# Optimization experiments

Hardware: AMD Instinct MI355X
Metric: run time of the kernel (lower is better)

Reference implementation:

```python
import jax, jax.numpy as jnp
import numpy as np

# ---- configuration (matches init_kwargs) ----
S = 128          # sheet_units
AK = 21          # aff_cf_units
AC = 2           # aff_cf_channels
AD = 1           # aff_cf_dilation
LK = 41          # lat_cf_units
LD = 1           # lat_cf_dilation
EX = 9           # exc_units
ITERS = 5        # lat_iters
STRENGTH = 1.5
MAX_INH = 1.0
MAX_R = 19       # oddenise(2*exc_units)


def _dist(size):
    c = (size - 1) / 2.0
    r = jnp.arange(size, dtype=jnp.float32) - c
    return jnp.sqrt(r[:, None] ** 2 + r[None, :] ** 2)


def get_circle(size, radius):
    return (_dist(size) < radius).astype(jnp.float32)


def get_radial_cos(size, period):
    return jnp.cos(_dist(size) * jnp.pi / period)


def unfold(x, k, dil=1):
    # x: (N,C,H,W) -> (N, C*k*k, L); channel-major patch order (same as torch F.unfold)
    p = jax.lax.conv_general_dilated_patches(
        x, (k, k), (1, 1), 'VALID', rhs_dilation=(dil, dil))
    return p.reshape(p.shape[0], p.shape[1], -1)


def setup_inputs() -> dict:
    key = jax.random.key(0)
    k1, k2, k3 = jax.random.split(key, 3)
    # afferent receptive-field envelope
    env = get_radial_cos(AK, AK) ** 2 * get_circle(AK, AK / 2)
    env = env / env.max()
    aff_cf_envelope = jnp.tile(env[None, None], (1, AC, 1, 1)).reshape(1, AC * AK * AK, 1)
    # short-range excitation kernel (normalised to sum 1)
    sre = get_radial_cos(EX, EX) ** 2 * get_circle(EX, EX / 2)
    sre = (sre / sre.sum())[None, None]  # (1,1,EX,EX)
    # lateral-inhibition envelope (annulus: full cutoff minus excitatory core)
    inh_mask = get_radial_cos(LK, EX / LD) ** 2 * get_circle(LK, EX / (2 * LD))
    lri = get_radial_cos(LK, LK) ** 2 * get_circle(LK, LK / 2) * (1.0 - inh_mask)
    lri_envelope = lri.reshape(1, LK * LK, 1)
    lri_envelope = lri_envelope / lri_envelope.max()
    # circular mask for the masked max-pool
    max_mask = get_circle(MAX_R, MAX_R / 2).reshape(1, MAX_R * MAX_R, 1)
    # parameters (init as in the module, jittered so they are not degenerate)
    P = AC * AK * AK
    K = LK * LK
    rfs = jnp.ones((S * S, P, 1), jnp.float32) * aff_cf_envelope
    rfs = rfs * jax.random.uniform(k1, rfs.shape, jnp.float32, 0.5, 1.5)
    rfs = rfs / (rfs.sum(1, keepdims=True) / P)
    lat_weights = jnp.ones((S * S, K, 1), jnp.float32) * lri_envelope
    lat_weights = lat_weights * jax.random.uniform(k2, lat_weights.shape, jnp.float32, 0.5, 1.5)
    lat_weights = lat_weights / (lat_weights.sum(1, keepdims=True) / K)
    adathresh = jnp.full((1, 1, S, S), 0.1, jnp.float32)
    H = S + (AK - 1) * AD  # 148: unfold must yield S x S output locations
    x = jax.random.uniform(k3, (1, AC, H, H), jnp.float32)
    return {"x": x, "rfs": rfs, "lat_weights": lat_weights, "adathresh": adathresh,
            "aff_cf_envelope": aff_cf_envelope, "sre": sre,
            "lri_envelope": lri_envelope, "max_mask": max_mask}


def reference(x, rfs, lat_weights, adathresh, aff_cf_envelope, sre, lri_envelope, max_mask):
    P = rfs.shape[1]
    K = lat_weights.shape[1]
    # weight renormalisation (done under no_grad in torch)
    rfs = rfs / (rfs.sum(1, keepdims=True) / P)
    lat_weights = lat_weights / (lat_weights.sum(1, keepdims=True) / K)
    lat_w = jax.lax.stop_gradient(lat_weights)[:, :, 0] / K          # (L,K)
    env_k = lri_envelope[0, :, 0]                                     # (K,)
    mmask = max_mask[0, :, 0]                                         # (M,)
    # afferent drive: locally connected (non-shared weight) receptive fields
    x_tiles = unfold(x, AK, AD) * aff_cf_envelope                     # (1,P,L)
    x_tiles = jnp.transpose(x_tiles, (2, 0, 1))                       # (L,1,P)
    raw_aff = jnp.einsum('lp,lp->l', x_tiles[:, 0, :], rfs[:, :, 0]).reshape(1, 1, S, S)
    aff = jax.lax.stop_gradient(raw_aff) / P - adathresh
    lat = jax.nn.relu(aff)
    lat_mean = jnp.zeros_like(lat)
    pos_pad = EX // 2
    pad = LK // 2 * LD
    max_pad = MAX_R // 2
    for _ in range(ITERS):
        # short-range excitation: shared-weight conv with reflect padding
        latp = jnp.pad(lat, ((0, 0), (0, 0), (pos_pad, pos_pad), (pos_pad, pos_pad)), mode='reflect')
        lat = jax.lax.conv_general_dilated(latp, sre, (1, 1), 'VALID',
                                           dimension_numbers=('NCHW', 'OIHW', 'NCHW'))
        # locally connected lateral inhibition (zero padding)
        latz = jnp.pad(lat, ((0, 0), (0, 0), (pad, pad), (pad, pad)))
        tiles = unfold(latz, LK, LD)[0].T * env_k                     # (L,K)
        lat_neg = jnp.einsum('lk,lk->l', tiles, lat_w).reshape(1, 1, S, S)
        lat = lat - lat_neg * MAX_INH
        lat = jax.nn.relu(lat + aff) * STRENGTH
        # masked local max normalisation (reflect padding)
        latr = jnp.pad(lat, ((0, 0), (0, 0), (max_pad, max_pad), (max_pad, max_pad)), mode='reflect')
        mtiles = unfold(latr, MAX_R)[0] * mmask[:, None]              # (M,L)
        lat_max = jnp.maximum(mtiles.max(0), 1.0).reshape(1, 1, S, S)
        lat = lat / (lat_max + 1e-5)
        lat_mean = lat_mean + lat
    lat_mean = lat_mean / ITERS
    # Hebbian-style lateral correlation objective (grads flow to lat_weights)
    lmz = jnp.pad(lat_mean, ((0, 0), (0, 0), (pad, pad), (pad, pad)))
    mtiles2 = unfold(lmz, LK, LD)[0].T * env_k                        # (L,K)
    lat_correlations = jnp.einsum('lk,lk,l->', mtiles2, lat_weights[:, :, 0],
                                  lat_mean.reshape(-1))
    return raw_aff, lat, lat_correlations, x_tiles
```

## Files before the change

### kernel.cpp

```cpp
#include <hip/hip_runtime.h>

#define S 128
#define L (S*S)
#define AK 21
#define AC 2
#define PP 882
#define HX 148
#define LK 41
#define KK 1681
#define EX 9
#define MAXR 19
#define NITER 5


__device__ __forceinline__ int reflect_idx(int i) {
  i = (i < 0) ? -i : i;
  return (i >= S) ? (2 * S - 2 - i) : i;
}

__device__ __forceinline__ void wave_red2(float& a, float& b) {
#pragma unroll
  for (int o = 32; o; o >>= 1) {
    a += __shfl_down(a, o);
    b += __shfl_down(b, o);
  }
}

__device__ __forceinline__ float gmap(const float* __restrict__ m,
                                      int i, int j, int kh, int kw) {
  int ii = i + kh - LK / 2;
  int jj = j + kw - LK / 2;
  return ((unsigned)ii < (unsigned)S && (unsigned)jj < (unsigned)S)
             ? m[ii * S + jj] : 0.f;
}

__device__ __forceinline__ void row_scan(const float* __restrict__ lw,
                                         const float* __restrict__ envk,
                                         const float* __restrict__ m,
                                         int wid, int lane,
                                         float& accn, float& accw) {
  int i = wid >> 7, j = wid & (S - 1);
  const float* wrow = lw + (size_t)wid * KK;
  const int pro = (4 - (wid & 3)) & 3;
  const int n4 = (KK - pro) >> 2;
  const int tail = (KK - pro) & 3;
  accn = 0.f; accw = 0.f;
  if (lane < pro) {
    int k = lane;
    float w = wrow[k];
    int kh = k / LK, kw = k - kh * LK;
    accw += w;
    accn += w * envk[k] * gmap(m, i, j, kh, kw);
  }
  const float4* wrow4 = (const float4*)(wrow + pro);
  for (int q = lane; q < n4; q += 64) {
    float4 w4 = wrow4[q];
    int k0 = pro + (q << 2);
    int kh = k0 / LK;
    int kw = k0 - kh * LK;
    accw += (w4.x + w4.y) + (w4.z + w4.w);
    float a;
    a = w4.x * envk[k0]     * gmap(m, i, j, kh, kw);
    kw++; if (kw >= LK) { kw -= LK; kh++; }
    a += w4.y * envk[k0 + 1] * gmap(m, i, j, kh, kw);
    kw++; if (kw >= LK) { kw -= LK; kh++; }
    a += w4.z * envk[k0 + 2] * gmap(m, i, j, kh, kw);
    kw++; if (kw >= LK) { kw -= LK; kh++; }
    a += w4.w * envk[k0 + 3] * gmap(m, i, j, kh, kw);
    accn += a;
  }
  if (lane < tail) {
    int k = pro + (n4 << 2) + lane;
    float w = wrow[k];
    int kh = k / LK, kw = k - kh * LK;
    accw += w;
    accn += w * envk[k] * gmap(m, i, j, kh, kw);
  }
  wave_red2(accn, accw);
}

__global__ void k_xtiles(const float* __restrict__ x,
                         const float* __restrict__ rfs,
                         const float* __restrict__ adath,
                         const float* __restrict__ aenv,
                         float* __restrict__ out_raw,
                         float* __restrict__ out_xt,
                         float* __restrict__ aff,
                         float* __restrict__ latA,
                         float* __restrict__ mean) {
  int wid = (blockIdx.x * blockDim.x + threadIdx.x) >> 6;
  int lane = threadIdx.x & 63;
  if (wid >= L) return;
  int i = wid >> 7, j = wid & (S - 1);
  const float2* rrow2 = (const float2*)(rfs + (size_t)wid * PP);
  float2* xrow2 = (float2*)(out_xt + (size_t)wid * PP);
  const float2* aenv2 = (const float2*)aenv;
  float accd = 0.f, accs = 0.f;
  for (int q = lane; q < PP / 2; q += 64) {
    float2 w2 = rrow2[q];
    float2 e2 = aenv2[q];
    int p0 = q << 1;
    int c = (p0 >= 441) ? 1 : 0;
    int r = p0 - c * 441;
    int kh = r / AK, kw = r - kh * AK;
    float xt0 = x[c * (HX * HX) + (i + kh) * HX + (j + kw)] * e2.x;
    int p1 = p0 + 1;
    int c1 = (p1 >= 441) ? 1 : 0;
    int r1 = p1 - c1 * 441;
    int kh1 = r1 / AK, kw1 = r1 - kh1 * AK;
    float xt1 = x[c1 * (HX * HX) + (i + kh1) * HX + (j + kw1)] * e2.y;
    xrow2[q] = make_float2(xt0, xt1);
    accd += xt0 * w2.x + xt1 * w2.y;
    accs += w2.x + w2.y;
  }
  wave_red2(accd, accs);
  if (lane == 0) {
    out_raw[wid] = accd * ((float)PP / accs);
    float a = accd / accs - adath[wid];
    aff[wid] = a;
    latA[wid] = a > 0.f ? a : 0.f;
    mean[wid] = 0.f;
  }
}

__global__ void k_conv(const float* __restrict__ latA,
                       const float* __restrict__ sre,
                       float* __restrict__ latC) {
  int wid = (blockIdx.x * blockDim.x + threadIdx.x) >> 6;
  int lane = threadIdx.x & 63;
  if (wid >= L) return;
  int i = wid >> 7, j = wid & (S - 1);
  float acc = 0.f;
#pragma unroll
  for (int t0 = 0; t0 < 2; ++t0) {
    int t = t0 * 64 + lane;
    if (t < EX * EX) {
      int u = t / EX, v = t - u * EX;
      int ii = reflect_idx(i + u - EX / 2);
      int jj = reflect_idx(j + v - EX / 2);
      acc += latA[ii * S + jj] * sre[t];
    }
  }
#pragma unroll
  for (int o = 32; o; o >>= 1) acc += __shfl_xor(acc, o);
  if (lane == 0) latC[wid] = acc;
}

__global__ void k_latneg(const float* __restrict__ lw,
                         const float* __restrict__ envk,
                         const float* __restrict__ latC,
                         const float* __restrict__ aff,
                         float* __restrict__ lat2) {
  int wid = (blockIdx.x * blockDim.x + threadIdx.x) >> 6;
  int lane = threadIdx.x & 63;
  if (wid >= L) return;
  float accn, accw;
  row_scan(lw, envk, latC, wid, lane, accn, accw);
  if (lane == 0) {
    float ln = accn / accw;
    float v = latC[wid] - ln + aff[wid];
    lat2[wid] = (v > 0.f ? v : 0.f) * 1.5f;
  }
}

__global__ void k_maxnorm(const float* __restrict__ lat2,
                          const float* __restrict__ mmask,
                          float* __restrict__ latA,
                          float* __restrict__ mean,
                          float* __restrict__ out_lat,
                          int last) {
  int wid = (blockIdx.x * blockDim.x + threadIdx.x) >> 6;
  int lane = threadIdx.x & 63;
  if (wid >= L) return;
  int i = wid >> 7, j = wid & (S - 1);
  float m = 1.0f;
#pragma unroll
  for (int t0 = 0; t0 < 6; ++t0) {
    int t = t0 * 64 + lane;
    if (t < MAXR * MAXR) {
      int u = t / MAXR, v = t - u * MAXR;
      int ii = reflect_idx(i + u - MAXR / 2);
      int jj = reflect_idx(j + v - MAXR / 2);
      m = fmaxf(m, lat2[ii * S + jj] * mmask[t]);
    }
  }
#pragma unroll
  for (int o = 32; o; o >>= 1) m = fmaxf(m, __shfl_xor(m, o));
  if (lane == 0) {
    float lv = lat2[wid] / (m + 1e-5f);
    latA[wid] = lv;
    mean[wid] += lv;
    if (last) out_lat[wid] = lv;
  }
}

__global__ void k_corrpart(const float* __restrict__ lw,
                           const float* __restrict__ envk,
                           const float* __restrict__ mean,
                           float* __restrict__ part) {
  int wid = (blockIdx.x * blockDim.x + threadIdx.x) >> 6;
  int lane = threadIdx.x & 63;
  if (wid >= L) return;
  float accn, accw;
  row_scan(lw, envk, mean, wid, lane, accn, accw);
  if (lane == 0) {
    const float inv_it = 1.0f / (float)NITER;
    float lm = mean[wid] * inv_it;
    part[wid] = lm * ((float)KK / accw) * (accn * inv_it);
  }
}

__global__ void k_reduce(const float* __restrict__ part,
                         float* __restrict__ out) {
  float a = 0.f;
  for (int idx = threadIdx.x; idx < L; idx += 256) a += part[idx];
#pragma unroll
  for (int o = 32; o; o >>= 1) a += __shfl_down(a, o);
  __shared__ float sm[4];
  if ((threadIdx.x & 63) == 0) sm[threadIdx.x >> 6] = a;
  __syncthreads();
  if (threadIdx.x == 0) out[0] = sm[0] + sm[1] + sm[2] + sm[3];
}

extern "C" void kernel_launch(void* const* d_in, const int* in_sizes, int n_in,
                              void* d_out, int out_size, void* d_ws, size_t ws_size,
                              hipStream_t stream) {
  const float* x     = (const float*)d_in[0];
  const float* rfs   = (const float*)d_in[1];
  const float* lw    = (const float*)d_in[2];
  const float* adath = (const float*)d_in[3];
  const float* aenv  = (const float*)d_in[4];
  const float* sre   = (const float*)d_in[5];
  const float* envk  = (const float*)d_in[6];
  const float* mmask = (const float*)d_in[7];

  float* out = (float*)d_out;
  float* out_raw = out;
  float* out_lat = out + L;
  float* out_cor = out + 2 * L;
  float* out_xt  = out + 2 * L + 1;

  float* wsf  = (float*)d_ws;
  float* aff  = wsf;
  float* latA = wsf + L;
  float* latC = wsf + 2 * L;
  float* lat2 = wsf + 3 * L;
  float* mean = wsf + 4 * L;
  float* part = wsf + 5 * L;

  dim3 blk(256);
  dim3 grid_wave(L / 4);

  k_xtiles<<<grid_wave, blk, 0, stream>>>(x, rfs, adath, aenv,
                                          out_raw, out_xt, aff, latA, mean);
  for (int it = 0; it < NITER; ++it) {
    k_conv<<<grid_wave, blk, 0, stream>>>(latA, sre, latC);
    k_latneg<<<grid_wave, blk, 0, stream>>>(lw, envk, latC, aff, lat2);
    k_maxnorm<<<grid_wave, blk, 0, stream>>>(lat2, mmask, latA, mean, out_lat,
                                             (it == NITER - 1) ? 1 : 0);
  }
  k_corrpart<<<grid_wave, blk, 0, stream>>>(lw, envk, mean, part);
  k_reduce<<<1, blk, 0, stream>>>(part, out_cor);
}
```

Baseline: 565.7 us.

## Transpose lateral weights once and compute inhibition with coalesced column-major passes

Adds a one-time transpose of the lateral weight matrix into workspace, fused with per-row weight sums. New latneg and correlation kernels read it k-major, so consecutive lanes read consecutive output positions. Taps with a zero envelope and out-of-bounds rows are skipped. The final reduction is folded in with an atomic add. This needs a large workspace and falls back to the old path otherwise, and the transpose adds a full extra read and write of the weights.

```diff
diff --git a/kernel.cpp b/kernel.cpp
--- a/kernel.cpp
+++ b/kernel.cpp
@@ -11,6 +11,7 @@
 #define EX 9
 #define MAXR 19
 #define NITER 5
+#define NW 16
 
 
 __device__ __forceinline__ int reflect_idx(int i) {
@@ -34,49 +35,33 @@
              ? m[ii * S + jj] : 0.f;
 }
 
-__device__ __forceinline__ void row_scan(const float* __restrict__ lw,
-                                         const float* __restrict__ envk,
-                                         const float* __restrict__ m,
-                                         int wid, int lane,
-                                         float& accn, float& accw) {
-  int i = wid >> 7, j = wid & (S - 1);
-  const float* wrow = lw + (size_t)wid * KK;
-  const int pro = (4 - (wid & 3)) & 3;
-  const int n4 = (KK - pro) >> 2;
-  const int tail = (KK - pro) & 3;
-  accn = 0.f; accw = 0.f;
-  if (lane < pro) {
-    int k = lane;
-    float w = wrow[k];
-    int kh = k / LK, kw = k - kh * LK;
-    accw += w;
-    accn += w * envk[k] * gmap(m, i, j, kh, kw);
-  }
-  const float4* wrow4 = (const float4*)(wrow + pro);
-  for (int q = lane; q < n4; q += 64) {
-    float4 w4 = wrow4[q];
-    int k0 = pro + (q << 2);
-    int kh = k0 / LK;
-    int kw = k0 - kh * LK;
-    accw += (w4.x + w4.y) + (w4.z + w4.w);
-    float a;
-    a = w4.x * envk[k0]     * gmap(m, i, j, kh, kw);
-    kw++; if (kw >= LK) { kw -= LK; kh++; }
-    a += w4.y * envk[k0 + 1] * gmap(m, i, j, kh, kw);
-    kw++; if (kw >= LK) { kw -= LK; kh++; }
-    a += w4.z * envk[k0 + 2] * gmap(m, i, j, kh, kw);
-    kw++; if (kw >= LK) { kw -= LK; kh++; }
-    a += w4.w * envk[k0 + 3] * gmap(m, i, j, kh, kw);
-    accn += a;
-  }
-  if (lane < tail) {
-    int k = pro + (n4 << 2) + lane;
-    float w = wrow[k];
-    int kh = k / LK, kw = k - kh * LK;
-    accw += w;
-    accn += w * envk[k] * gmap(m, i, j, kh, kw);
-  }
-  wave_red2(accn, accw);
+__global__ void k_transpose(const float* __restrict__ lw,
+                            float* __restrict__ lwT,
+                            float* __restrict__ wsum) {
+  __shared__ float tile[64][65];
+  int kt = blockIdx.x;
+  int lt = blockIdx.y;
+  int tid = threadIdx.x;
+  int c = tid & 63, r0 = tid >> 6;
+#pragma unroll
+  for (int p = 0; p < 16; ++p) {
+    int r = r0 + (p << 2);
+    int k = kt * 64 + c;
+    int l = lt * 64 + r;
+    tile[r][c] = (k < KK) ? lw[(size_t)l * KK + k] : 0.f;
+  }
+  __syncthreads();
+  if (tid < 64) {
+    float s = 0.f;
+    for (int cc = 0; cc < 64; ++cc) s += tile[tid][cc];
+    atomicAdd(&wsum[lt * 64 + tid], s);
+  }
+#pragma unroll
+  for (int p = 0; p < 16; ++p) {
+    int rr = r0 + (p << 2);
+    int k = kt * 64 + rr;
+    if (k < KK) lwT[(size_t)k * L + lt * 64 + c] = tile[c][rr];
+  }
 }
 
 __global__ void k_xtiles(const float* __restrict__ x,
@@ -146,6 +131,161 @@
   if (lane == 0) latC[wid] = acc;
 }
 
+__global__ __launch_bounds__(1024)
+void k_latneg_t(const float* __restrict__ lwT,
+                const float* __restrict__ wsum,
+                const float* __restrict__ envk,
+                const float* __restrict__ latC,
+                const float* __restrict__ aff,
+                float* __restrict__ lat2) {
+  int b = blockIdx.x;
+  int tid = threadIdx.x;
+  int wave = tid >> 6, lane = tid & 63;
+  int l0 = b << 6;
+  int i = l0 >> 7;
+  int jb = (b & 1) << 6;
+  float acc = 0.f;
+  for (int k = wave; k < KK; k += NW) {
+    float ek = envk[k];
+    if (ek == 0.f) continue;
+    int kh = k / LK, kw = k - kh * LK;
+    int ii = i + kh - LK / 2;
+    if ((unsigned)ii >= (unsigned)S) continue;
+    int jj = jb + kw - LK / 2 + lane;
+    float pv = ((unsigned)jj < (unsigned)S) ? latC[ii * S + jj] : 0.f;
+    acc += lwT[(size_t)k * L + l0 + lane] * ek * pv;
+  }
+  __shared__ float red[NW][64];
+  red[wave][lane] = acc;
+  __syncthreads();
+  if (wave == 0) {
+    float s = 0.f;
+#pragma unroll
+    for (int w = 0; w < NW; ++w) s += red[w][lane];
+    int l = l0 + lane;
+    float ln = s / wsum[l];
+    float v = latC[l] - ln + aff[l];
+    lat2[l] = (v > 0.f ? v : 0.f) * 1.5f;
+  }
+}
+
+__global__ void k_maxnorm(const float* __restrict__ lat2,
+                          const float* __restrict__ mmask,
+                          float* __restrict__ latA,
+                          float* __restrict__ mean,
+                          float* __restrict__ out_lat,
+                          int last) {
+  int wid = (blockIdx.x * blockDim.x + threadIdx.x) >> 6;
+  int lane = threadIdx.x & 63;
+  if (wid >= L) return;
+  int i = wid >> 7, j = wid & (S - 1);
+  float m = 1.0f;
+#pragma unroll
+  for (int t0 = 0; t0 < 6; ++t0) {
+    int t = t0 * 64 + lane;
+    if (t < MAXR * MAXR) {
+      int u = t / MAXR, v = t - u * MAXR;
+      int ii = reflect_idx(i + u - MAXR / 2);
+      int jj = reflect_idx(j + v - MAXR / 2);
+      m = fmaxf(m, lat2[ii * S + jj] * mmask[t]);
+    }
+  }
+#pragma unroll
+  for (int o = 32; o; o >>= 1) m = fmaxf(m, __shfl_xor(m, o));
+  if (lane == 0) {
+    float lv = lat2[wid] / (m + 1e-5f);
+    latA[wid] = lv;
+    mean[wid] += lv;
+    if (last) out_lat[wid] = lv;
+  }
+}
+
+__global__ __launch_bounds__(1024)
+void k_corr_t(const float* __restrict__ lwT,
+              const float* __restrict__ wsum,
+              const float* __restrict__ envk,
+              const float* __restrict__ mean,
+              float* __restrict__ out_cor) {
+  int b = blockIdx.x;
+  int tid = threadIdx.x;
+  int wave = tid >> 6, lane = tid & 63;
+  int l0 = b << 6;
+  int i = l0 >> 7;
+  int jb = (b & 1) << 6;
+  float acc = 0.f;
+  for (int k = wave; k < KK; k += NW) {
+    float ek = envk[k];
+    if (ek == 0.f) continue;
+    int kh = k / LK, kw = k - kh * LK;
+    int ii = i + kh - LK / 2;
+    if ((unsigned)ii >= (unsigned)S) continue;
+    int jj = jb + kw - LK / 2 + lane;
+    float pv = ((unsigned)jj < (unsigned)S) ? mean[ii * S + jj] : 0.f;
+    acc += lwT[(size_t)k * L + l0 + lane] * ek * pv;
+  }
+  __shared__ float red[NW][64];
+  red[wave][lane] = acc;
+  __syncthreads();
+  if (wave == 0) {
+    float s = 0.f;
+#pragma unroll
+    for (int w = 0; w < NW; ++w) s += red[w][lane];
+    int l = l0 + lane;
+    const float inv_it = 1.0f / (float)NITER;
+    float lm = mean[l] * inv_it;
+    float c = lm * ((float)KK / wsum[l]) * (s * inv_it);
+#pragma unroll
+    for (int o = 32; o; o >>= 1) c += __shfl_down(c, o);
+    if (lane == 0) atomicAdd(out_cor, c);
+  }
+}
+
+
+__device__ __forceinline__ void row_scan(const float* __restrict__ lw,
+                                         const float* __restrict__ envk,
+                                         const float* __restrict__ m,
+                                         int wid, int lane,
+                                         float& accn, float& accw) {
+  int i = wid >> 7, j = wid & (S - 1);
+  const float* wrow = lw + (size_t)wid * KK;
+  const int pro = (4 - (wid & 3)) & 3;
+  const int n4 = (KK - pro) >> 2;
+  const int tail = (KK - pro) & 3;
+  accn = 0.f; accw = 0.f;
+  if (lane < pro) {
+    int k = lane;
+    float w = wrow[k];
+    int kh = k / LK, kw = k - kh * LK;
+    accw += w;
+    accn += w * envk[k] * gmap(m, i, j, kh, kw);
+  }
+  const float4* wrow4 = (const float4*)(wrow + pro);
+  for (int q = lane; q < n4; q += 64) {
+    float4 w4 = wrow4[q];
+    int k0 = pro + (q << 2);
+    int kh = k0 / LK;
+    int kw = k0 - kh * LK;
+    accw += (w4.x + w4.y) + (w4.z + w4.w);
+    float a;
+    a = w4.x * envk[k0]     * gmap(m, i, j, kh, kw);
+    kw++; if (kw >= LK) { kw -= LK; kh++; }
+    a += w4.y * envk[k0 + 1] * gmap(m, i, j, kh, kw);
+    kw++; if (kw >= LK) { kw -= LK; kh++; }
+    a += w4.z * envk[k0 + 2] * gmap(m, i, j, kh, kw);
+    kw++; if (kw >= LK) { kw -= LK; kh++; }
+    a += w4.w * envk[k0 + 3] * gmap(m, i, j, kh, kw);
+    accn += a;
+  }
+  if (lane < tail) {
+    int k = pro + (n4 << 2) + lane;
+    float w = wrow[k];
+    int kh = k / LK, kw = k - kh * LK;
+    accw += w;
+    accn += w * envk[k] * gmap(m, i, j, kh, kw);
+  }
+  wave_red2(accn, accw);
+}
+
 __global__ void k_latneg(const float* __restrict__ lw,
                          const float* __restrict__ envk,
                          const float* __restrict__ latC,
@@ -163,37 +303,6 @@
   }
 }
 
-__global__ void k_maxnorm(const float* __restrict__ lat2,
-                          const float* __restrict__ mmask,
-                          float* __restrict__ latA,
-                          float* __restrict__ mean,
-                          float* __restrict__ out_lat,
-                          int last) {
-  int wid = (blockIdx.x * blockDim.x + threadIdx.x) >> 6;
-  int lane = threadIdx.x & 63;
-  if (wid >= L) return;
-  int i = wid >> 7, j = wid & (S - 1);
-  float m = 1.0f;
-#pragma unroll
-  for (int t0 = 0; t0 < 6; ++t0) {
-    int t = t0 * 64 + lane;
-    if (t < MAXR * MAXR) {
-      int u = t / MAXR, v = t - u * MAXR;
-      int ii = reflect_idx(i + u - MAXR / 2);
-      int jj = reflect_idx(j + v - MAXR / 2);
-      m = fmaxf(m, lat2[ii * S + jj] * mmask[t]);
-    }
-  }
-#pragma unroll
-  for (int o = 32; o; o >>= 1) m = fmaxf(m, __shfl_xor(m, o));
-  if (lane == 0) {
-    float lv = lat2[wid] / (m + 1e-5f);
-    latA[wid] = lv;
-    mean[wid] += lv;
-    if (last) out_lat[wid] = lv;
-  }
-}
-
 __global__ void k_corrpart(const float* __restrict__ lw,
                            const float* __restrict__ envk,
                            const float* __restrict__ mean,
@@ -240,25 +349,54 @@
   float* out_cor = out + 2 * L;
   float* out_xt  = out + 2 * L + 1;
 
-  float* wsf  = (float*)d_ws;
-  float* aff  = wsf;
-  float* latA = wsf + L;
-  float* latC = wsf + 2 * L;
-  float* lat2 = wsf + 3 * L;
-  float* mean = wsf + 4 * L;
-  float* part = wsf + 5 * L;
-
   dim3 blk(256);
   dim3 grid_wave(L / 4);
 
-  k_xtiles<<<grid_wave, blk, 0, stream>>>(x, rfs, adath, aenv,
-                                          out_raw, out_xt, aff, latA, mean);
-  for (int it = 0; it < NITER; ++it) {
-    k_conv<<<grid_wave, blk, 0, stream>>>(latA, sre, latC);
-    k_latneg<<<grid_wave, blk, 0, stream>>>(lw, envk, latC, aff, lat2);
-    k_maxnorm<<<grid_wave, blk, 0, stream>>>(lat2, mmask, latA, mean, out_lat,
-                                             (it == NITER - 1) ? 1 : 0);
-  }
-  k_corrpart<<<grid_wave, blk, 0, stream>>>(lw, envk, mean, part);
-  k_reduce<<<1, blk, 0, stream>>>(part, out_cor);
-}
+  size_t need = ((size_t)KK * L + 8 * (size_t)L) * sizeof(float);
+
+  if (ws_size >= need) {
+    float* wsf  = (float*)d_ws;
+    float* lwT  = wsf;
+    float* wsum = wsf + (size_t)KK * L;
+    float* aff  = wsum + L;
+    float* latA = aff + L;
+    float* latC = latA + L;
+    float* lat2 = latC + L;
+    float* mean = lat2 + L;
+
+    hipMemsetAsync(wsum, 0, L * sizeof(float), stream);
+    hipMemsetAsync(out_cor, 0, sizeof(float), stream);
+
+    k_transpose<<<dim3(27, 256), blk, 0, stream>>>(lw, lwT, wsum);
+    k_xtiles<<<grid_wave, blk, 0, stream>>>(x, rfs, adath, aenv,
+                                            out_raw, out_xt, aff, latA, mean);
+    for (int it = 0; it < NITER; ++it) {
+      k_conv<<<grid_wave, blk, 0, stream>>>(latA, sre, latC);
+      k_latneg_t<<<dim3(L / 64), dim3(64 * NW), 0, stream>>>(lwT, wsum, envk,
+                                                             latC, aff, lat2);
+      k_maxnorm<<<grid_wave, blk, 0, stream>>>(lat2, mmask, latA, mean, out_lat,
+                                               (it == NITER - 1) ? 1 : 0);
+    }
+    k_corr_t<<<dim3(L / 64), dim3(64 * NW), 0, stream>>>(lwT, wsum, envk,
+                                                         mean, out_cor);
+  } else {
+    float* wsf  = (float*)d_ws;
+    float* aff  = wsf;
+    float* latA = wsf + L;
+    float* latC = wsf + 2 * L;
+    float* lat2 = wsf + 3 * L;
+    float* mean = wsf + 4 * L;
+    float* part = wsf + 5 * L;
+
+    k_xtiles<<<grid_wave, blk, 0, stream>>>(x, rfs, adath, aenv,
+                                            out_raw, out_xt, aff, latA, mean);
+    for (int it = 0; it < NITER; ++it) {
+      k_conv<<<grid_wave, blk, 0, stream>>>(latA, sre, latC);
+      k_latneg<<<grid_wave, blk, 0, stream>>>(lw, envk, latC, aff, lat2);
+      k_maxnorm<<<grid_wave, blk, 0, stream>>>(lat2, mmask, latA, mean, out_lat,
+                                               (it == NITER - 1) ? 1 : 0);
+    }
+    k_corrpart<<<grid_wave, blk, 0, stream>>>(lw, envk, mean, part);
+    k_reduce<<<1, blk, 0, stream>>>(part, out_cor);
+  }
+}
```

Result: slower. 683.4 us (+20.8%).
